# Performance work log

Measured on AMD Instinct MI355X. Metric: run time of the kernel, lower is better.

## Reference

```python
import jax, jax.numpy as jnp
import numpy as np

B, S, D, H = 2, 2048, 1024, 16
HD = D // H  # head_dim = 64
EPS = 1e-12


def setup_inputs() -> dict:
    key = jax.random.key(0)
    ks = jax.random.split(key, 12)
    s = 0.02
    return {
        "hidden_states": jax.random.normal(ks[0], (B, S, D), jnp.float32),
        "attention_mask": jnp.zeros((B, 1, 1, S), jnp.float32),
        "alibi_bias": jax.random.normal(ks[1], (1, H, S, S), jnp.float32) * 0.1,
        "Wq": jax.random.normal(ks[2], (D, D), jnp.float32) * s,
        "bq": jnp.zeros((D,), jnp.float32),
        "Wk": jax.random.normal(ks[3], (D, D), jnp.float32) * s,
        "bk": jnp.zeros((D,), jnp.float32),
        "Wv": jax.random.normal(ks[4], (D, D), jnp.float32) * s,
        "bv": jnp.zeros((D,), jnp.float32),
        "Wo": jax.random.normal(ks[5], (D, D), jnp.float32) * s,
        "bo": jnp.zeros((D,), jnp.float32),
        "ln_gamma": jnp.ones((D,), jnp.float32),
        "ln_beta": jnp.zeros((D,), jnp.float32),
    }


def _split_heads(x):
    # [B, S, D] -> [B, H, S, HD]
    return x.reshape(B, S, H, HD).transpose(0, 2, 1, 3)


def reference(hidden_states, attention_mask, alibi_bias,
              Wq, bq, Wk, bk, Wv, bv, Wo, bo, ln_gamma, ln_beta):
    q = _split_heads(hidden_states @ Wq + bq)
    k = _split_heads(hidden_states @ Wk + bk)
    v = _split_heads(hidden_states @ Wv + bv)

    scale = HD ** -0.5
    # combined additive mask: [B,1,1,S] + [1,H,S,S] -> broadcast [B,H,S,S]
    combined_mask = attention_mask + alibi_bias
    scores = jnp.einsum('bhqd,bhkd->bhqk', q, k) * scale + combined_mask
    probs = jax.nn.softmax(scores, axis=-1)
    attn = jnp.einsum('bhqk,bhkd->bhqd', probs, v)  # [B,H,S,HD]
    attn = attn.transpose(0, 2, 1, 3).reshape(B, S, D)

    out = attn @ Wo + bo
    x = hidden_states + out  # post-norm residual
    mu = jnp.mean(x, axis=-1, keepdims=True)
    var = jnp.mean(jnp.square(x - mu), axis=-1, keepdims=True)
    return (x - mu) * jax.lax.rsqrt(var + EPS) * ln_gamma + ln_beta
```

## Files before the change

kernel.cpp:

```cpp
#include <hip/hip_runtime.h>

#define Bb 2
#define Ss 2048
#define Dd 1024
#define Hh 16
#define HD 64
#define Mm (Bb*Ss)

typedef __bf16 bf16;
typedef __bf16 bf16x8 __attribute__((ext_vector_type(8)));
typedef float f32x4 __attribute__((ext_vector_type(4)));

__global__ void cvt_f32_bf16(const float* __restrict__ in, bf16* __restrict__ out, int n4) {
    int i = blockIdx.x * blockDim.x + threadIdx.x;
    if (i < n4) {
        float4 v = *(const float4*)(in + i * 4);
        out[i*4+0] = (bf16)v.x; out[i*4+1] = (bf16)v.y;
        out[i*4+2] = (bf16)v.z; out[i*4+3] = (bf16)v.w;
    }
}

__global__ void wtrans(const float* __restrict__ W0, const float* __restrict__ W1,
                       const float* __restrict__ W2, const float* __restrict__ W3,
                       bf16* __restrict__ O0, bf16* __restrict__ O1,
                       bf16* __restrict__ O2, bf16* __restrict__ O3) {
    const float* W = (blockIdx.z == 0) ? W0 : (blockIdx.z == 1) ? W1 : (blockIdx.z == 2) ? W2 : W3;
    bf16* O = (blockIdx.z == 0) ? O0 : (blockIdx.z == 1) ? O1 : (blockIdx.z == 2) ? O2 : O3;
    __shared__ bf16 t[64][65];
    int k0 = blockIdx.x * 64, n0 = blockIdx.y * 64;
    for (int c = threadIdx.x; c < 4096; c += 256) {
        int r = c >> 6, cc = c & 63;
        t[r][cc] = (bf16)W[(k0 + r) * Dd + n0 + cc];
    }
    __syncthreads();
    for (int c = threadIdx.x; c < 4096; c += 256) {
        int r = c >> 6, cc = c & 63;
        O[(n0 + r) * Dd + k0 + cc] = t[cc][r];
    }
}

__global__ __launch_bounds__(256, 2)
void gemm_bt(const bf16* __restrict__ A, const bf16* __restrict__ Bt,
             const float* __restrict__ bias, bf16* __restrict__ out, int mode) {
    const int K = 1024, N = 1024;
    __shared__ __align__(16) bf16 As[128 * 32];
    __shared__ __align__(16) bf16 Bs[128 * 32];
    int tid = threadIdx.x;
    int wave = tid >> 6, lane = tid & 63;
    int lane15 = lane & 15, quad = lane >> 4;
    int wm = (wave >> 1) * 64, wn = (wave & 1) * 64;
    int m0 = blockIdx.x * 128, n0 = blockIdx.y * 128;
    int srow = tid >> 2;
    int skoff = (tid & 3) * 8;

    f32x4 acc[4][4] = {};

    for (int kt = 0; kt < K; kt += 32) {
        __syncthreads();
        *(bf16x8*)(&As[srow * 32 + skoff])        = *(const bf16x8*)(&A[(m0 + srow) * K + kt + skoff]);
        *(bf16x8*)(&As[(srow + 64) * 32 + skoff]) = *(const bf16x8*)(&A[(m0 + srow + 64) * K + kt + skoff]);
        *(bf16x8*)(&Bs[srow * 32 + skoff])        = *(const bf16x8*)(&Bt[(n0 + srow) * K + kt + skoff]);
        *(bf16x8*)(&Bs[(srow + 64) * 32 + skoff]) = *(const bf16x8*)(&Bt[(n0 + srow + 64) * K + kt + skoff]);
        __syncthreads();
        bf16x8 af[4], bfr[4];
#pragma unroll
        for (int i = 0; i < 4; i++) af[i] = *(const bf16x8*)(&As[(wm + i * 16 + lane15) * 32 + quad * 8]);
#pragma unroll
        for (int j = 0; j < 4; j++) bfr[j] = *(const bf16x8*)(&Bs[(wn + j * 16 + lane15) * 32 + quad * 8]);
#pragma unroll
        for (int i = 0; i < 4; i++)
#pragma unroll
            for (int j = 0; j < 4; j++)
                acc[i][j] = __builtin_amdgcn_mfma_f32_16x16x32_bf16(af[i], bfr[j], acc[i][j], 0, 0, 0);
    }

#pragma unroll
    for (int i = 0; i < 4; i++) {
        int mbase = m0 + wm + i * 16 + quad * 4;
#pragma unroll
        for (int j = 0; j < 4; j++) {
            int n = n0 + wn + j * 16 + lane15;
            float bv = bias[n];
#pragma unroll
            for (int r = 0; r < 4; r++) {
                float v = acc[i][j][r] + bv;
                int m = mbase + r;
                if (mode == 0) {
                    out[m * N + n] = (bf16)v;
                } else {
                    int b = m >> 11, s = m & 2047, h = n >> 6, hd = n & 63;
                    out[(((size_t)(b * Hh + h) * Ss + s) * HD) + hd] = (bf16)v;
                }
            }
        }
    }
}

__global__ __launch_bounds__(256, 2)
void attn_kernel(const bf16* __restrict__ Q, const bf16* __restrict__ Kk, const bf16* __restrict__ V,
                 const float* __restrict__ alibi, const float* __restrict__ mask,
                 bf16* __restrict__ outattn) {
    int qt = blockIdx.x, h = blockIdx.y, b = blockIdx.z;
    __shared__ __align__(16) bf16 Qs[64 * 64];
    __shared__ __align__(16) bf16 Ks[64 * 64];
    __shared__ __align__(16) bf16 Vts[64 * 64];
    __shared__ __align__(16) bf16 Ps[64 * 64];
    int tid = threadIdx.x, wave = tid >> 6, lane = tid & 63;
    int lane15 = lane & 15, quad = lane >> 4;

    const bf16* Qbase = Q + ((size_t)(b * Hh + h) * Ss + qt * 64) * HD;
    const bf16* Kbase = Kk + (size_t)(b * Hh + h) * Ss * HD;
    const bf16* Vbase = V + (size_t)(b * Hh + h) * Ss * HD;

    for (int c = tid; c < 512; c += 256) {
        int r = c >> 3, off = (c & 7) * 8;
        *(bf16x8*)(&Qs[r * 64 + off]) = *(const bf16x8*)(&Qbase[r * HD + off]);
    }
    __syncthreads();
    bf16x8 qf0 = *(const bf16x8*)(&Qs[(wave * 16 + lane15) * 64 + quad * 8]);
    bf16x8 qf1 = *(const bf16x8*)(&Qs[(wave * 16 + lane15) * 64 + 32 + quad * 8]);

    float m_i[4], l_i[4];
    f32x4 O[4] = {};
#pragma unroll
    for (int r = 0; r < 4; r++) { m_i[r] = -1e30f; l_i[r] = 0.f; }

    const float scale = 0.125f;
    const float* alibi_base = alibi + ((size_t)h * Ss + qt * 64 + wave * 16 + quad * 4) * Ss;
    const float* mask_base = mask + b * Ss;

    for (int kt = 0; kt < Ss; kt += 64) {
        __syncthreads();
        for (int c = tid; c < 512; c += 256) {
            int r = c >> 3, off = (c & 7) * 8;
            *(bf16x8*)(&Ks[r * 64 + off]) = *(const bf16x8*)(&Kbase[(kt + r) * HD + off]);
        }
        for (int c = tid; c < 512; c += 256) {
            int r = c >> 3, off = (c & 7) * 8;
            bf16x8 v = *(const bf16x8*)(&Vbase[(kt + r) * HD + off]);
#pragma unroll
            for (int e = 0; e < 8; e++) Vts[(off + e) * 64 + r] = v[e];
        }
        __syncthreads();

        f32x4 sc[4];
        f32x4 z = {0.f, 0.f, 0.f, 0.f};
#pragma unroll
        for (int j = 0; j < 4; j++) {
            bf16x8 kf0 = *(const bf16x8*)(&Ks[(j * 16 + lane15) * 64 + quad * 8]);
            bf16x8 kf1 = *(const bf16x8*)(&Ks[(j * 16 + lane15) * 64 + 32 + quad * 8]);
            f32x4 s = __builtin_amdgcn_mfma_f32_16x16x32_bf16(qf0, kf0, z, 0, 0, 0);
            s = __builtin_amdgcn_mfma_f32_16x16x32_bf16(qf1, kf1, s, 0, 0, 0);
            sc[j] = s;
        }
#pragma unroll
        for (int j = 0; j < 4; j++) {
            int col = kt + j * 16 + lane15;
            float mk = mask_base[col];
#pragma unroll
            for (int r = 0; r < 4; r++) {
                float al = alibi_base[(size_t)r * Ss + col];
                sc[j][r] = sc[j][r] * scale + al + mk;
            }
        }
        float alpha[4];
#pragma unroll
        for (int r = 0; r < 4; r++) {
            float v = fmaxf(fmaxf(sc[0][r], sc[1][r]), fmaxf(sc[2][r], sc[3][r]));
#pragma unroll
            for (int d = 1; d < 16; d <<= 1) v = fmaxf(v, __shfl_xor(v, d, 64));
            float mnew = fmaxf(m_i[r], v);
            alpha[r] = __expf(m_i[r] - mnew);
            m_i[r] = mnew;
        }
        float rs[4] = {0.f, 0.f, 0.f, 0.f};
#pragma unroll
        for (int j = 0; j < 4; j++)
#pragma unroll
            for (int r = 0; r < 4; r++) {
                float p = __expf(sc[j][r] - m_i[r]);
                sc[j][r] = p;
                rs[r] += p;
            }
#pragma unroll
        for (int r = 0; r < 4; r++) {
            float v = rs[r];
#pragma unroll
            for (int d = 1; d < 16; d <<= 1) v += __shfl_xor(v, d, 64);
            l_i[r] = l_i[r] * alpha[r] + v;
        }
#pragma unroll
        for (int j = 0; j < 4; j++)
#pragma unroll
            for (int r = 0; r < 4; r++)
                Ps[(wave * 16 + quad * 4 + r) * 64 + j * 16 + lane15] = (bf16)sc[j][r];
        __syncthreads();

        bf16x8 pf0 = *(const bf16x8*)(&Ps[(wave * 16 + lane15) * 64 + quad * 8]);
        bf16x8 pf1 = *(const bf16x8*)(&Ps[(wave * 16 + lane15) * 64 + 32 + quad * 8]);
#pragma unroll
        for (int jd = 0; jd < 4; jd++) {
#pragma unroll
            for (int r = 0; r < 4; r++) O[jd][r] *= alpha[r];
            bf16x8 vf0 = *(const bf16x8*)(&Vts[(jd * 16 + lane15) * 64 + quad * 8]);
            bf16x8 vf1 = *(const bf16x8*)(&Vts[(jd * 16 + lane15) * 64 + 32 + quad * 8]);
            O[jd] = __builtin_amdgcn_mfma_f32_16x16x32_bf16(pf0, vf0, O[jd], 0, 0, 0);
            O[jd] = __builtin_amdgcn_mfma_f32_16x16x32_bf16(pf1, vf1, O[jd], 0, 0, 0);
        }
    }

#pragma unroll
    for (int jd = 0; jd < 4; jd++) {
        int d = jd * 16 + lane15;
#pragma unroll
        for (int r = 0; r < 4; r++) {
            int qg = qt * 64 + wave * 16 + quad * 4 + r;
            float v = O[jd][r] / l_i[r];
            outattn[(((size_t)b * Ss + qg) * Hh + h) * HD + d] = (bf16)v;
        }
    }
}

__global__ void ln_kernel(const float* __restrict__ hidden, const bf16* __restrict__ Y,
                          const float* __restrict__ gamma, const float* __restrict__ beta,
                          float* __restrict__ out) {
    int row = blockIdx.x;
    int tid = threadIdx.x, wave = tid >> 6, lane = tid & 63;
    float x[4];
    float s = 0.f, q = 0.f;
#pragma unroll
    for (int e = 0; e < 4; e++) {
        int col = e * 256 + tid;
        x[e] = hidden[(size_t)row * Dd + col] + (float)Y[(size_t)row * Dd + col];
        s += x[e];
        q += x[e] * x[e];
    }
#pragma unroll
    for (int d = 1; d < 64; d <<= 1) { s += __shfl_xor(s, d, 64); q += __shfl_xor(q, d, 64); }
    __shared__ float sm[4], sq[4];
    if (lane == 0) { sm[wave] = s; sq[wave] = q; }
    __syncthreads();
    float tot = sm[0] + sm[1] + sm[2] + sm[3];
    float totq = sq[0] + sq[1] + sq[2] + sq[3];
    float mu = tot * (1.f / 1024.f);
    float var = totq * (1.f / 1024.f) - mu * mu;
    float rstd = rsqrtf(var + 1e-12f);
#pragma unroll
    for (int e = 0; e < 4; e++) {
        int col = e * 256 + tid;
        out[(size_t)row * Dd + col] = (x[e] - mu) * rstd * gamma[col] + beta[col];
    }
}

extern "C" void kernel_launch(void* const* d_in, const int* in_sizes, int n_in,
                              void* d_out, int out_size, void* d_ws, size_t ws_size,
                              hipStream_t stream) {
    const float* hidden = (const float*)d_in[0];
    const float* amask  = (const float*)d_in[1];
    const float* alibi  = (const float*)d_in[2];
    const float* Wq = (const float*)d_in[3];
    const float* bq = (const float*)d_in[4];
    const float* Wk = (const float*)d_in[5];
    const float* bk = (const float*)d_in[6];
    const float* Wv = (const float*)d_in[7];
    const float* bv = (const float*)d_in[8];
    const float* Wo = (const float*)d_in[9];
    const float* bo = (const float*)d_in[10];
    const float* ln_g = (const float*)d_in[11];
    const float* ln_b = (const float*)d_in[12];
    float* out = (float*)d_out;

    char* w = (char*)d_ws;
    bf16* Xb   = (bf16*)(w);
    bf16* WqT  = (bf16*)(w + 8388608);
    bf16* WkT  = (bf16*)(w + 10485760);
    bf16* WvT  = (bf16*)(w + 12582912);
    bf16* WoT  = (bf16*)(w + 14680064);
    bf16* Qw   = (bf16*)(w + 16777216);
    bf16* Kw   = (bf16*)(w + 25165824);
    bf16* Vw   = (bf16*)(w + 33554432);
    bf16* Attn = (bf16*)(w + 41943040);
    bf16* Yw   = (bf16*)(w + 50331648);

    cvt_f32_bf16<<<4096, 256, 0, stream>>>(hidden, Xb, Mm * Dd / 4);
    wtrans<<<dim3(16, 16, 4), 256, 0, stream>>>(Wq, Wk, Wv, Wo, WqT, WkT, WvT, WoT);

    gemm_bt<<<dim3(32, 8), 256, 0, stream>>>(Xb, WqT, bq, Qw, 1);
    gemm_bt<<<dim3(32, 8), 256, 0, stream>>>(Xb, WkT, bk, Kw, 1);
    gemm_bt<<<dim3(32, 8), 256, 0, stream>>>(Xb, WvT, bv, Vw, 1);

    attn_kernel<<<dim3(32, 16, 2), 256, 0, stream>>>(Qw, Kw, Vw, alibi, amask, Attn);

    gemm_bt<<<dim3(32, 8), 256, 0, stream>>>(Attn, WoT, bo, Yw, 0);

    ln_kernel<<<4096, 256, 0, stream>>>(hidden, Yw, ln_g, ln_b, out);
}
```

Before: 650.0 us.

## Fuse QKV GEMMs, use direct global-to-LDS loads, swizzle attention LDS, stage alibi

The three Q/K/V projection GEMMs become a single launch with a 3x wider N grid. This relies on the transposed weights sitting contiguously in the workspace and picks the per-tile bias and output pointer. GEMM tile loads now use global_load_lds, so data goes straight from global memory to LDS without passing through registers, and occupancy hints are raised. In the attention kernel, the Q/P, K and transposed V tiles use XOR-swizzled LDS layouts to cut bank conflicts, Q and P share one buffer, and each alibi tile is loaded with coalesced float4 reads into a swizzled LDS buffer instead of strided per-lane global reads. The trade-off is more LDS per block and more index arithmetic.

```diff
diff --git a/kernel.cpp b/kernel.cpp
--- a/kernel.cpp
+++ b/kernel.cpp
@@ -10,6 +10,13 @@
 typedef __bf16 bf16;
 typedef __bf16 bf16x8 __attribute__((ext_vector_type(8)));
 typedef float f32x4 __attribute__((ext_vector_type(4)));
+
+__device__ __forceinline__ void gload_lds16(const bf16* g, bf16* l) {
+    __builtin_amdgcn_global_load_lds(
+        (const __attribute__((address_space(1))) unsigned int*)g,
+        (__attribute__((address_space(3))) unsigned int*)l,
+        16, 0, 0);
+}
 
 __global__ void cvt_f32_bf16(const float* __restrict__ in, bf16* __restrict__ out, int n4) {
     int i = blockIdx.x * blockDim.x + threadIdx.x;
@@ -39,10 +46,11 @@
     }
 }
 
-__global__ __launch_bounds__(256, 2)
+__global__ __launch_bounds__(256, 3)
 void gemm_bt(const bf16* __restrict__ A, const bf16* __restrict__ Bt,
-             const float* __restrict__ bias, bf16* __restrict__ out, int mode) {
-    const int K = 1024, N = 1024;
+             const float* __restrict__ b0, const float* __restrict__ b1, const float* __restrict__ b2,
+             bf16* __restrict__ o0, bf16* __restrict__ o1, bf16* __restrict__ o2, int mode) {
+    const int K = 1024;
     __shared__ __align__(16) bf16 As[128 * 32];
     __shared__ __align__(16) bf16 Bs[128 * 32];
     int tid = threadIdx.x;
@@ -50,17 +58,20 @@
     int lane15 = lane & 15, quad = lane >> 4;
     int wm = (wave >> 1) * 64, wn = (wave & 1) * 64;
     int m0 = blockIdx.x * 128, n0 = blockIdx.y * 128;
-    int srow = tid >> 2;
-    int skoff = (tid & 3) * 8;
+    int lrow = lane >> 2, lcol = (lane & 3) * 8;
+    const bf16* Ag = &A[(size_t)(m0 + wave * 16 + lrow) * K + lcol];
+    const bf16* Bg = &Bt[(size_t)(n0 + wave * 16 + lrow) * K + lcol];
+    bf16* Asw = &As[wave * 16 * 32];
+    bf16* Bsw = &Bs[wave * 16 * 32];
 
     f32x4 acc[4][4] = {};
 
     for (int kt = 0; kt < K; kt += 32) {
         __syncthreads();
-        *(bf16x8*)(&As[srow * 32 + skoff])        = *(const bf16x8*)(&A[(m0 + srow) * K + kt + skoff]);
-        *(bf16x8*)(&As[(srow + 64) * 32 + skoff]) = *(const bf16x8*)(&A[(m0 + srow + 64) * K + kt + skoff]);
-        *(bf16x8*)(&Bs[srow * 32 + skoff])        = *(const bf16x8*)(&Bt[(n0 + srow) * K + kt + skoff]);
-        *(bf16x8*)(&Bs[(srow + 64) * 32 + skoff]) = *(const bf16x8*)(&Bt[(n0 + srow + 64) * K + kt + skoff]);
+        gload_lds16(Ag + kt,           Asw);
+        gload_lds16(Ag + 64 * K + kt,  Asw + 64 * 32);
+        gload_lds16(Bg + kt,           Bsw);
+        gload_lds16(Bg + 64 * K + kt,  Bsw + 64 * 32);
         __syncthreads();
         bf16x8 af[4], bfr[4];
 #pragma unroll
@@ -80,45 +91,54 @@
 #pragma unroll
         for (int j = 0; j < 4; j++) {
             int n = n0 + wn + j * 16 + lane15;
-            float bv = bias[n];
-#pragma unroll
-            for (int r = 0; r < 4; r++) {
-                float v = acc[i][j][r] + bv;
-                int m = mbase + r;
-                if (mode == 0) {
-                    out[m * N + n] = (bf16)v;
-                } else {
-                    int b = m >> 11, s = m & 2047, h = n >> 6, hd = n & 63;
-                    out[(((size_t)(b * Hh + h) * Ss + s) * HD) + hd] = (bf16)v;
+            if (mode == 0) {
+                float bv = b0[n];
+#pragma unroll
+                for (int r = 0; r < 4; r++)
+                    o0[(size_t)(mbase + r) * 1024 + n] = (bf16)(acc[i][j][r] + bv);
+            } else {
+                int which = n >> 10, nn = n & 1023;
+                const float* bp = (which == 0) ? b0 : (which == 1) ? b1 : b2;
+                bf16* op = (which == 0) ? o0 : (which == 1) ? o1 : o2;
+                float bv = bp[nn];
+                int hh = nn >> 6, hd = nn & 63;
+#pragma unroll
+                for (int r = 0; r < 4; r++) {
+                    int m = mbase + r;
+                    int bb = m >> 11, s = m & 2047;
+                    op[(((size_t)(bb * Hh + hh) * Ss + s) * HD) + hd] = (bf16)(acc[i][j][r] + bv);
                 }
             }
         }
     }
 }
 
-__global__ __launch_bounds__(256, 2)
+__global__ __launch_bounds__(256, 4)
 void attn_kernel(const bf16* __restrict__ Q, const bf16* __restrict__ Kk, const bf16* __restrict__ V,
                  const float* __restrict__ alibi, const float* __restrict__ mask,
                  bf16* __restrict__ outattn) {
     int qt = blockIdx.x, h = blockIdx.y, b = blockIdx.z;
-    __shared__ __align__(16) bf16 Qs[64 * 64];
     __shared__ __align__(16) bf16 Ks[64 * 64];
     __shared__ __align__(16) bf16 Vts[64 * 64];
-    __shared__ __align__(16) bf16 Ps[64 * 64];
+    __shared__ __align__(16) bf16 QPs[64 * 64];
+    __shared__ __align__(16) float Als[64 * 64];
     int tid = threadIdx.x, wave = tid >> 6, lane = tid & 63;
     int lane15 = lane & 15, quad = lane >> 4;
 
     const bf16* Qbase = Q + ((size_t)(b * Hh + h) * Ss + qt * 64) * HD;
     const bf16* Kbase = Kk + (size_t)(b * Hh + h) * Ss * HD;
     const bf16* Vbase = V + (size_t)(b * Hh + h) * Ss * HD;
+    const float* Abase = alibi + ((size_t)h * Ss + qt * 64) * Ss;
+    const float* mask_base = mask + (size_t)b * Ss;
 
     for (int c = tid; c < 512; c += 256) {
         int r = c >> 3, off = (c & 7) * 8;
-        *(bf16x8*)(&Qs[r * 64 + off]) = *(const bf16x8*)(&Qbase[r * HD + off]);
+        *(bf16x8*)(&QPs[r * 64 + (off ^ ((r & 7) * 8))]) = *(const bf16x8*)(&Qbase[r * HD + off]);
     }
     __syncthreads();
-    bf16x8 qf0 = *(const bf16x8*)(&Qs[(wave * 16 + lane15) * 64 + quad * 8]);
-    bf16x8 qf1 = *(const bf16x8*)(&Qs[(wave * 16 + lane15) * 64 + 32 + quad * 8]);
+    int qrow = wave * 16 + lane15;
+    bf16x8 qf0 = *(const bf16x8*)(&QPs[qrow * 64 + ((quad * 8) ^ ((qrow & 7) * 8))]);
+    bf16x8 qf1 = *(const bf16x8*)(&QPs[qrow * 64 + ((32 + quad * 8) ^ ((qrow & 7) * 8))]);
 
     float m_i[4], l_i[4];
     f32x4 O[4] = {};
@@ -126,20 +146,26 @@
     for (int r = 0; r < 4; r++) { m_i[r] = -1e30f; l_i[r] = 0.f; }
 
     const float scale = 0.125f;
-    const float* alibi_base = alibi + ((size_t)h * Ss + qt * 64 + wave * 16 + quad * 4) * Ss;
-    const float* mask_base = mask + b * Ss;
 
     for (int kt = 0; kt < Ss; kt += 64) {
         __syncthreads();
         for (int c = tid; c < 512; c += 256) {
             int r = c >> 3, off = (c & 7) * 8;
-            *(bf16x8*)(&Ks[r * 64 + off]) = *(const bf16x8*)(&Kbase[(kt + r) * HD + off]);
+            *(bf16x8*)(&Ks[r * 64 + (off ^ ((r & 7) * 8))]) = *(const bf16x8*)(&Kbase[(size_t)(kt + r) * HD + off]);
         }
         for (int c = tid; c < 512; c += 256) {
             int r = c >> 3, off = (c & 7) * 8;
-            bf16x8 v = *(const bf16x8*)(&Vbase[(kt + r) * HD + off]);
-#pragma unroll
-            for (int e = 0; e < 8; e++) Vts[(off + e) * 64 + r] = v[e];
+            bf16x8 v = *(const bf16x8*)(&Vbase[(size_t)(kt + r) * HD + off]);
+#pragma unroll
+            for (int e = 0; e < 8; e++) {
+                int d = off + e;
+                Vts[d * 64 + (r ^ ((((d & 7) ^ ((d >> 3) & 7))) * 8))] = v[e];
+            }
+        }
+        for (int c = tid; c < 1024; c += 256) {
+            int r = c >> 4, c4 = (c & 15) * 4;
+            *(float4*)(&Als[r * 64 + (c4 ^ (((r >> 2) & 1) * 16 + ((r >> 3) & 1) * 8))]) =
+                *(const float4*)(&Abase[(size_t)r * Ss + kt + c4]);
         }
         __syncthreads();
 
@@ -147,19 +173,21 @@
         f32x4 z = {0.f, 0.f, 0.f, 0.f};
 #pragma unroll
         for (int j = 0; j < 4; j++) {
-            bf16x8 kf0 = *(const bf16x8*)(&Ks[(j * 16 + lane15) * 64 + quad * 8]);
-            bf16x8 kf1 = *(const bf16x8*)(&Ks[(j * 16 + lane15) * 64 + 32 + quad * 8]);
+            int krow = j * 16 + lane15;
+            bf16x8 kf0 = *(const bf16x8*)(&Ks[krow * 64 + ((quad * 8) ^ ((krow & 7) * 8))]);
+            bf16x8 kf1 = *(const bf16x8*)(&Ks[krow * 64 + ((32 + quad * 8) ^ ((krow & 7) * 8))]);
             f32x4 s = __builtin_amdgcn_mfma_f32_16x16x32_bf16(qf0, kf0, z, 0, 0, 0);
             s = __builtin_amdgcn_mfma_f32_16x16x32_bf16(qf1, kf1, s, 0, 0, 0);
             sc[j] = s;
         }
 #pragma unroll
         for (int j = 0; j < 4; j++) {
-            int col = kt + j * 16 + lane15;
-            float mk = mask_base[col];
+            int col = j * 16 + lane15;
+            float mk = mask_base[kt + col];
 #pragma unroll
             for (int r = 0; r < 4; r++) {
-                float al = alibi_base[(size_t)r * Ss + col];
+                int row = wave * 16 + quad * 4 + r;
+                float al = Als[row * 64 + (col ^ (((row >> 2) & 1) * 16 + ((row >> 3) & 1) * 8))];
                 sc[j][r] = sc[j][r] * scale + al + mk;
             }
         }
@@ -192,18 +220,23 @@
 #pragma unroll
         for (int j = 0; j < 4; j++)
 #pragma unroll
-            for (int r = 0; r < 4; r++)
-                Ps[(wave * 16 + quad * 4 + r) * 64 + j * 16 + lane15] = (bf16)sc[j][r];
-        __syncthreads();
-
-        bf16x8 pf0 = *(const bf16x8*)(&Ps[(wave * 16 + lane15) * 64 + quad * 8]);
-        bf16x8 pf1 = *(const bf16x8*)(&Ps[(wave * 16 + lane15) * 64 + 32 + quad * 8]);
+            for (int r = 0; r < 4; r++) {
+                int row = wave * 16 + quad * 4 + r;
+                QPs[row * 64 + ((j * 16 + lane15) ^ ((row & 7) * 8))] = (bf16)sc[j][r];
+            }
+        __syncthreads();
+
+        int prow = wave * 16 + lane15;
+        bf16x8 pf0 = *(const bf16x8*)(&QPs[prow * 64 + ((quad * 8) ^ ((prow & 7) * 8))]);
+        bf16x8 pf1 = *(const bf16x8*)(&QPs[prow * 64 + ((32 + quad * 8) ^ ((prow & 7) * 8))]);
 #pragma unroll
         for (int jd = 0; jd < 4; jd++) {
+            int vrow = jd * 16 + lane15;
+            int vs = (((vrow & 7) ^ ((vrow >> 3) & 7)) * 8);
 #pragma unroll
             for (int r = 0; r < 4; r++) O[jd][r] *= alpha[r];
-            bf16x8 vf0 = *(const bf16x8*)(&Vts[(jd * 16 + lane15) * 64 + quad * 8]);
-            bf16x8 vf1 = *(const bf16x8*)(&Vts[(jd * 16 + lane15) * 64 + 32 + quad * 8]);
+            bf16x8 vf0 = *(const bf16x8*)(&Vts[vrow * 64 + ((quad * 8) ^ vs)]);
+            bf16x8 vf1 = *(const bf16x8*)(&Vts[vrow * 64 + ((32 + quad * 8) ^ vs)]);
             O[jd] = __builtin_amdgcn_mfma_f32_16x16x32_bf16(pf0, vf0, O[jd], 0, 0, 0);
             O[jd] = __builtin_amdgcn_mfma_f32_16x16x32_bf16(pf1, vf1, O[jd], 0, 0, 0);
         }
@@ -285,13 +318,11 @@
     cvt_f32_bf16<<<4096, 256, 0, stream>>>(hidden, Xb, Mm * Dd / 4);
     wtrans<<<dim3(16, 16, 4), 256, 0, stream>>>(Wq, Wk, Wv, Wo, WqT, WkT, WvT, WoT);
 
-    gemm_bt<<<dim3(32, 8), 256, 0, stream>>>(Xb, WqT, bq, Qw, 1);
-    gemm_bt<<<dim3(32, 8), 256, 0, stream>>>(Xb, WkT, bk, Kw, 1);
-    gemm_bt<<<dim3(32, 8), 256, 0, stream>>>(Xb, WvT, bv, Vw, 1);
+    gemm_bt<<<dim3(32, 24), 256, 0, stream>>>(Xb, WqT, bq, bk, bv, Qw, Kw, Vw, 1);
 
     attn_kernel<<<dim3(32, 16, 2), 256, 0, stream>>>(Qw, Kw, Vw, alibi, amask, Attn);
 
-    gemm_bt<<<dim3(32, 8), 256, 0, stream>>>(Attn, WoT, bo, Yw, 0);
+    gemm_bt<<<dim3(32, 8), 256, 0, stream>>>(Attn, WoT, bo, nullptr, nullptr, Yw, nullptr, nullptr, 0);
 
     ln_kernel<<<4096, 256, 0, stream>>>(hidden, Yw, ln_g, ln_b, out);
 }
```

Result: faster. 637.1 us (-2.0%).
